# Optimization experiments

Measured on AMD Instinct MI355X. Metric: run time of the kernel, lower is better.

## Reference

```python
import jax, jax.numpy as jnp
import numpy as np
import math

IN_F = 2048
INTER_F = 8192
OUT_F = 2048
STRIPE = 256
N_STRIPES = INTER_F // STRIPE
EPS = 1e-7
BETA = 0.99
STEPS = 1000.0
THRESH_LR_SCALE = 1.0 * math.sqrt(IN_F)


def setup_inputs() -> dict:
    key = jax.random.key(0)
    ks = jax.random.split(key, 8)
    x = jax.random.normal(ks[0], (2, 1024, IN_F), dtype=jnp.float32)
    gate_weight = jax.random.normal(ks[1], (IN_F, INTER_F), dtype=jnp.float32) / math.sqrt(IN_F)
    gate_bias = jnp.zeros((INTER_F,), dtype=jnp.float32)
    # thresholds ~ threshold_init scale so the mask is non-trivially sparse
    gate_thresholds = jax.random.uniform(ks[2], (N_STRIPES, IN_F), dtype=jnp.float32) * (0.1 / THRESH_LR_SCALE) * 20.0
    med = jax.random.normal(ks[3], (IN_F,), dtype=jnp.float32) * 0.01
    aad = jax.random.uniform(ks[4], (IN_F,), dtype=jnp.float32) + 0.5
    up_weight = jax.random.normal(ks[5], (IN_F, INTER_F), dtype=jnp.float32) * 0.02
    up_bias = jnp.zeros((INTER_F,), dtype=jnp.float32)
    down_weight = jax.random.normal(ks[6], (OUT_F, INTER_F), dtype=jnp.float32) / math.sqrt(INTER_F)
    down_bias = jnp.zeros((OUT_F,), dtype=jnp.float32)
    return dict(x=x, gate_weight=gate_weight, gate_bias=gate_bias,
                gate_thresholds=gate_thresholds, med=med, aad=aad,
                up_weight=up_weight, up_bias=up_bias,
                down_weight=down_weight, down_bias=down_bias)


def _cwic_linear(xf, weight, bias, thresholds, med, aad):
    # eval-mode CWICLinear. xf: [T, I]
    debiaser = 1.0 / (EPS + (1.0 - BETA ** STEPS))
    mu = med * debiaser                                   # [I]
    std = aad * debiaser / math.sqrt(2.0 * math.pi)      # [I]
    thr = thresholds * std[None, :] * THRESH_LR_SCALE     # [N, I]
    xd = xf - mu[None, :]                                 # [T, I]
    mask = (jnp.abs(xd)[:, None, :] > thr[None]).astype(xf.dtype)  # [T, N, I]
    xm = xd[:, None, :] * mask + mu[None, None, :]        # [T, N, I]
    w = weight.T.reshape(N_STRIPES, STRIPE, IN_F)          # [N, S, I]
    y = jnp.einsum('nsi,tni->tns', w, xm).reshape(-1, INTER_F) + bias[None, :]
    active = STRIPE * mask.reshape(xf.shape[0], -1).sum(axis=-1)  # [T]
    dense = jnp.full_like(active, STRIPE * N_STRIPES * IN_F)
    return y, dense, active


def reference(x, gate_weight, gate_bias, gate_thresholds, med, aad,
              up_weight, up_bias, down_weight, down_bias):
    B, T, I = x.shape
    xf = x.reshape(-1, I)
    g, dense, active = _cwic_linear(xf, gate_weight, gate_bias, gate_thresholds, med, aad)
    up = xf @ up_weight + up_bias[None, :]                 # Conv1D: x @ W + b
    h = jax.nn.silu(g) * up                                # [BT, inter]
    y = h @ down_weight.T + down_bias[None, :]             # nn.Linear
    return (y.reshape(B, T, OUT_F), dense.reshape(B, T), active.reshape(B, T))
```

## Files before the change

kernel.cpp:

```cpp
#include <hip/hip_runtime.h>
#include <math.h>
#include <stdint.h>

typedef __bf16 bf16_t;
typedef __bf16 bf16x8 __attribute__((ext_vector_type(8)));
typedef __bf16 bf16x4 __attribute__((ext_vector_type(4)));
typedef float f32x4 __attribute__((ext_vector_type(4)));
typedef short s16x8 __attribute__((ext_vector_type(8)));

#define TOKS 2048
#define INF 2048
#define JNF 8192
#define ONF 2048


template <int ROWS, int NT>
__device__ __forceinline__ void stage_async_t(const bf16_t* __restrict__ src, size_t ld,
                                              bf16_t* lds, int tid) {
  constexpr int IT = ROWS * 8 / NT;
#pragma unroll
  for (int r = 0; r < IT; ++r) {
    int c = r * NT + tid;
    int row = c >> 3;
    int kq = (c & 7) ^ (row & 7);
    const bf16_t* g = src + (size_t)row * ld + kq * 8;
    bf16_t* l = lds + (size_t)(r * NT + (tid & ~63)) * 8;
    __builtin_amdgcn_global_load_lds((const __attribute__((address_space(1))) void*)g,
                                     (__attribute__((address_space(3))) void*)l,
                                     16, 0, 0);
  }
}

__device__ __forceinline__ bf16x8 frag_ld64(const bf16_t* lds, int row, int kq) {
  int slot = kq ^ (row & 7);
  return *(const bf16x8*)&lds[row * 64 + slot * 8];
}


__global__ __launch_bounds__(256) void prep_mu_thr(
    const float* __restrict__ med, const float* __restrict__ aad,
    const float* __restrict__ gth, float debiaser,
    float* __restrict__ mu, float* __restrict__ thr, bf16_t* __restrict__ thrb) {
  int gid = blockIdx.x * 256 + threadIdx.x;
  if (gid < INF) mu[gid] = med[gid] * debiaser;
  int i = gid & (INF - 1);
  float stdv = aad[i] * debiaser / 2.5066282746310002f;
  float tv = gth[gid] * stdv * 45.254833995939045f;
  thr[gid] = tv;
  thrb[gid] = (bf16_t)tv;
}

__global__ __launch_bounds__(256) void prep_x_count(
    const float* __restrict__ x, const float* __restrict__ mu,
    const float* __restrict__ thr,
    bf16_t* __restrict__ xb, bf16_t* __restrict__ xdb,
    float* __restrict__ dense, float* __restrict__ active) {
  int t = blockIdx.x;
  int tid = threadIdx.x;
  int i0 = tid * 8;
  const float* xrow = x + (size_t)t * INF;
  f32x4 x0 = *(const f32x4*)&xrow[i0];
  f32x4 x1 = *(const f32x4*)&xrow[i0 + 4];
  f32x4 m0 = *(const f32x4*)&mu[i0];
  f32x4 m1 = *(const f32x4*)&mu[i0 + 4];
  f32x4 d0 = x0 - m0, d1 = x1 - m1;
  bf16x8 ox, od;
  ox[0] = (bf16_t)x0[0]; ox[1] = (bf16_t)x0[1]; ox[2] = (bf16_t)x0[2]; ox[3] = (bf16_t)x0[3];
  ox[4] = (bf16_t)x1[0]; ox[5] = (bf16_t)x1[1]; ox[6] = (bf16_t)x1[2]; ox[7] = (bf16_t)x1[3];
  od[0] = (bf16_t)d0[0]; od[1] = (bf16_t)d0[1]; od[2] = (bf16_t)d0[2]; od[3] = (bf16_t)d0[3];
  od[4] = (bf16_t)d1[0]; od[5] = (bf16_t)d1[1]; od[6] = (bf16_t)d1[2]; od[7] = (bf16_t)d1[3];
  *(bf16x8*)&xb[(size_t)t * INF + i0] = ox;
  *(bf16x8*)&xdb[(size_t)t * INF + i0] = od;
  f32x4 a0, a1;
  a0[0] = fabsf(d0[0]); a0[1] = fabsf(d0[1]); a0[2] = fabsf(d0[2]); a0[3] = fabsf(d0[3]);
  a1[0] = fabsf(d1[0]); a1[1] = fabsf(d1[1]); a1[2] = fabsf(d1[2]); a1[3] = fabsf(d1[3]);
  int cnt = 0;
#pragma unroll 4
  for (int n = 0; n < 32; ++n) {
    f32x4 t0 = *(const f32x4*)&thr[(n << 11) + i0];
    f32x4 t1 = *(const f32x4*)&thr[(n << 11) + i0 + 4];
    cnt += (a0[0] > t0[0]) + (a0[1] > t0[1]) + (a0[2] > t0[2]) + (a0[3] > t0[3]);
    cnt += (a1[0] > t1[0]) + (a1[1] > t1[1]) + (a1[2] > t1[2]) + (a1[3] > t1[3]);
  }
  for (int off = 32; off; off >>= 1) cnt += __shfl_down(cnt, off);
  __shared__ int red[4];
  int wv = tid >> 6;
  if ((tid & 63) == 0) red[wv] = cnt;
  __syncthreads();
  if (tid == 0) {
    int tot = red[0] + red[1] + red[2] + red[3];
    active[t] = 256.0f * (float)tot;
    dense[t] = 16777216.0f;
  }
}

__global__ __launch_bounds__(256) void transpose_cast_dual(
    const float* __restrict__ src0, bf16_t* __restrict__ dst0,
    const float* __restrict__ src1, bf16_t* __restrict__ dst1) {
  const float* src = blockIdx.z ? src1 : src0;
  bf16_t* dst = blockIdx.z ? dst1 : dst0;
  __shared__ float tile[32][33];
  int j0 = blockIdx.x * 32;
  int i0 = blockIdx.y * 32;
  int r = threadIdx.x >> 3;
  int c = (threadIdx.x & 7) * 4;
  f32x4 v = *(const f32x4*)&src[(i0 + r) * JNF + j0 + c];
  tile[r][c] = v[0]; tile[r][c + 1] = v[1]; tile[r][c + 2] = v[2]; tile[r][c + 3] = v[3];
  __syncthreads();
  bf16x4 o;
  o[0] = (bf16_t)tile[c + 0][r];
  o[1] = (bf16_t)tile[c + 1][r];
  o[2] = (bf16_t)tile[c + 2][r];
  o[3] = (bf16_t)tile[c + 3][r];
  *(bf16x4*)&dst[(j0 + r) * INF + i0 + c] = o;
}

__global__ __launch_bounds__(256) void cast_bf16(
    const float* __restrict__ src, bf16_t* __restrict__ dst) {
  int idx = (blockIdx.x * 256 + threadIdx.x) * 8;
  f32x4 a = *(const f32x4*)&src[idx];
  f32x4 b = *(const f32x4*)&src[idx + 4];
  bf16x8 o;
  o[0] = (bf16_t)a[0]; o[1] = (bf16_t)a[1]; o[2] = (bf16_t)a[2]; o[3] = (bf16_t)a[3];
  o[4] = (bf16_t)b[0]; o[5] = (bf16_t)b[1]; o[6] = (bf16_t)b[2]; o[7] = (bf16_t)b[3];
  *(bf16x8*)&dst[idx] = o;
}

__global__ __launch_bounds__(256) void c_from_gwT(
    const bf16_t* __restrict__ gwT, const float* __restrict__ mu,
    const float* __restrict__ gb, float* __restrict__ c) {
  int j = blockIdx.x * 4 + (threadIdx.x >> 6);
  int lane = threadIdx.x & 63;
  float s = 0.f;
#pragma unroll
  for (int it = 0; it < 4; ++it) {
    int i = it * 512 + lane * 8;
    bf16x8 w = *(const bf16x8*)&gwT[(size_t)j * INF + i];
    f32x4 m0 = *(const f32x4*)&mu[i];
    f32x4 m1 = *(const f32x4*)&mu[i + 4];
    s += (float)w[0] * m0[0] + (float)w[1] * m0[1] + (float)w[2] * m0[2] + (float)w[3] * m0[3];
    s += (float)w[4] * m1[0] + (float)w[5] * m1[1] + (float)w[6] * m1[2] + (float)w[7] * m1[3];
  }
  for (int off = 32; off; off >>= 1) s += __shfl_down(s, off);
  if (lane == 0) c[j] = gb[j] + s;
}


__global__ __launch_bounds__(512) void gate_gemm(
    const bf16_t* __restrict__ xdb, const bf16_t* __restrict__ thrb,
    const bf16_t* __restrict__ gwT, const float* __restrict__ cj,
    bf16_t* __restrict__ g) {
  __shared__ bf16_t Al[128 * 64];
  __shared__ bf16_t Bl[256 * 64];
  int tid = threadIdx.x;
  int t0 = blockIdx.y * 128;
  int j0 = blockIdx.x * 256;
  int n = blockIdx.x;
  int lane = tid & 63;
  int wv = tid >> 6;
  int wr = (wv & 1) * 64;
  int wc = (wv >> 1) * 64;
  int m16 = lane & 15, q = lane >> 4;
  f32x4 acc[4][4] = {};
  const s16x8 absmask = {0x7FFF, 0x7FFF, 0x7FFF, 0x7FFF, 0x7FFF, 0x7FFF, 0x7FFF, 0x7FFF};
  for (int k0 = 0; k0 < INF; k0 += 64) {
    stage_async_t<256, 512>(gwT + (size_t)j0 * INF + k0, INF, Bl, tid);
#pragma unroll
    for (int r = 0; r < 2; ++r) {
      int c = r * 512 + tid;
      int row = c >> 3;
      int slot = c & 7;
      int kq = slot ^ (row & 7);
      s16x8 a = *(const s16x8*)&xdb[(size_t)(t0 + row) * INF + k0 + kq * 8];
      s16x8 t = *(const s16x8*)&thrb[n * INF + k0 + kq * 8];
      s16x8 m = (s16x8)((t - (a & absmask)) >> 15);
      *(s16x8*)&Al[row * 64 + slot * 8] = a & m;
    }
    __syncthreads();
#pragma unroll
    for (int s = 0; s < 2; ++s) {
      bf16x8 af[4], bf[4];
#pragma unroll
      for (int mi = 0; mi < 4; ++mi) af[mi] = frag_ld64(Al, wr + mi * 16 + m16, s * 4 + q);
#pragma unroll
      for (int ni = 0; ni < 4; ++ni) bf[ni] = frag_ld64(Bl, wc + ni * 16 + m16, s * 4 + q);
#pragma unroll
      for (int mi = 0; mi < 4; ++mi)
#pragma unroll
        for (int ni = 0; ni < 4; ++ni)
          acc[mi][ni] = __builtin_amdgcn_mfma_f32_16x16x32_bf16(af[mi], bf[ni], acc[mi][ni], 0, 0, 0);
    }
    __syncthreads();
  }
#pragma unroll
  for (int mi = 0; mi < 4; ++mi)
#pragma unroll
    for (int ni = 0; ni < 4; ++ni) {
      int col = j0 + wc + ni * 16 + m16;
      float cadd = cj[col];
#pragma unroll
      for (int r = 0; r < 4; ++r) {
        int row = t0 + wr + mi * 16 + q * 4 + r;
        g[(size_t)row * JNF + col] = (bf16_t)(acc[mi][ni][r] + cadd);
      }
    }
}


__global__ __launch_bounds__(256) void up_gemm(
    const bf16_t* __restrict__ xb, const bf16_t* __restrict__ upT,
    const float* __restrict__ ub, const bf16_t* __restrict__ g,
    bf16_t* __restrict__ h) {
  __shared__ bf16_t Al[128 * 64];
  __shared__ bf16_t Bl[128 * 64];
  int tid = threadIdx.x;
  int t0 = blockIdx.y * 128;
  int j0 = blockIdx.x * 128;
  int lane = tid & 63;
  int wv = tid >> 6;
  int wr = (wv & 1) * 64;
  int wc = (wv >> 1) * 64;
  int m16 = lane & 15, q = lane >> 4;
  f32x4 acc[4][4] = {};
  for (int k0 = 0; k0 < INF; k0 += 64) {
    stage_async_t<128, 256>(xb + (size_t)t0 * INF + k0, INF, Al, tid);
    stage_async_t<128, 256>(upT + (size_t)j0 * INF + k0, INF, Bl, tid);
    __syncthreads();
#pragma unroll
    for (int s = 0; s < 2; ++s) {
      bf16x8 af[4], bf[4];
#pragma unroll
      for (int mi = 0; mi < 4; ++mi) af[mi] = frag_ld64(Al, wr + mi * 16 + m16, s * 4 + q);
#pragma unroll
      for (int ni = 0; ni < 4; ++ni) bf[ni] = frag_ld64(Bl, wc + ni * 16 + m16, s * 4 + q);
#pragma unroll
      for (int mi = 0; mi < 4; ++mi)
#pragma unroll
        for (int ni = 0; ni < 4; ++ni)
          acc[mi][ni] = __builtin_amdgcn_mfma_f32_16x16x32_bf16(af[mi], bf[ni], acc[mi][ni], 0, 0, 0);
    }
    __syncthreads();
  }
#pragma unroll
  for (int mi = 0; mi < 4; ++mi)
#pragma unroll
    for (int ni = 0; ni < 4; ++ni) {
      int col = j0 + wc + ni * 16 + m16;
      float bias = ub[col];
#pragma unroll
      for (int r = 0; r < 4; ++r) {
        int row = t0 + wr + mi * 16 + q * 4 + r;
        float upv = acc[mi][ni][r] + bias;
        float gv = (float)g[(size_t)row * JNF + col];
        float hv = (gv / (1.f + expf(-gv))) * upv;
        h[(size_t)row * JNF + col] = (bf16_t)hv;
      }
    }
}

__global__ __launch_bounds__(256) void down_gemm(
    const bf16_t* __restrict__ h, const bf16_t* __restrict__ dwb,
    float* __restrict__ part) {
  __shared__ bf16_t Al[128 * 64];
  __shared__ bf16_t Bl[128 * 64];
  int tid = threadIdx.x;
  int t0 = blockIdx.y * 128;
  int o0 = blockIdx.x * 128;
  int kz = blockIdx.z * 2048;
  int lane = tid & 63;
  int wv = tid >> 6;
  int wr = (wv & 1) * 64;
  int wc = (wv >> 1) * 64;
  int m16 = lane & 15, q = lane >> 4;
  f32x4 acc[4][4] = {};
  for (int k0 = kz; k0 < kz + 2048; k0 += 64) {
    stage_async_t<128, 256>(h + (size_t)t0 * JNF + k0, JNF, Al, tid);
    stage_async_t<128, 256>(dwb + (size_t)o0 * JNF + k0, JNF, Bl, tid);
    __syncthreads();
#pragma unroll
    for (int s = 0; s < 2; ++s) {
      bf16x8 af[4], bf[4];
#pragma unroll
      for (int mi = 0; mi < 4; ++mi) af[mi] = frag_ld64(Al, wr + mi * 16 + m16, s * 4 + q);
#pragma unroll
      for (int ni = 0; ni < 4; ++ni) bf[ni] = frag_ld64(Bl, wc + ni * 16 + m16, s * 4 + q);
#pragma unroll
      for (int mi = 0; mi < 4; ++mi)
#pragma unroll
        for (int ni = 0; ni < 4; ++ni)
          acc[mi][ni] = __builtin_amdgcn_mfma_f32_16x16x32_bf16(af[mi], bf[ni], acc[mi][ni], 0, 0, 0);
    }
    __syncthreads();
  }
  float* dst = part + (size_t)blockIdx.z * (TOKS * ONF);
#pragma unroll
  for (int mi = 0; mi < 4; ++mi)
#pragma unroll
    for (int ni = 0; ni < 4; ++ni) {
      int col = o0 + wc + ni * 16 + m16;
#pragma unroll
      for (int r = 0; r < 4; ++r) {
        int row = t0 + wr + mi * 16 + q * 4 + r;
        dst[(size_t)row * ONF + col] = acc[mi][ni][r];
      }
    }
}

__global__ __launch_bounds__(256) void down_reduce(
    const float* __restrict__ part, const float* __restrict__ db,
    float* __restrict__ y) {
  int idx = (blockIdx.x * 256 + threadIdx.x) * 4;
  f32x4 a = *(const f32x4*)&part[idx];
  f32x4 b = *(const f32x4*)&part[idx + 4194304];
  f32x4 c = *(const f32x4*)&part[idx + 2 * 4194304];
  f32x4 d = *(const f32x4*)&part[idx + 3 * 4194304];
  f32x4 bias = *(const f32x4*)&db[idx & (ONF - 1)];
  *(f32x4*)&y[idx] = a + b + c + d + bias;
}


extern "C" void kernel_launch(void* const* d_in, const int* in_sizes, int n_in,
                              void* d_out, int out_size, void* d_ws, size_t ws_size,
                              hipStream_t stream) {
  (void)in_sizes; (void)n_in; (void)out_size; (void)ws_size;
  const float* x   = (const float*)d_in[0];
  const float* gw  = (const float*)d_in[1];
  const float* gb  = (const float*)d_in[2];
  const float* gth = (const float*)d_in[3];
  const float* med = (const float*)d_in[4];
  const float* aad = (const float*)d_in[5];
  const float* uw  = (const float*)d_in[6];
  const float* ub  = (const float*)d_in[7];
  const float* dw  = (const float*)d_in[8];
  const float* db  = (const float*)d_in[9];

  float* out = (float*)d_out;
  float* y = out;
  float* dense = out + 4194304;
  float* active = dense + 2048;

  char* ws = (char*)d_ws;
  float*  mu   = (float*)(ws + 0);
  float*  thr  = (float*)(ws + 8192);
  bf16_t* thrb = (bf16_t*)(ws + 270336);
  float*  cj   = (float*)(ws + 401408);
  bf16_t* xb   = (bf16_t*)(ws + 434176);
  bf16_t* xdb  = (bf16_t*)(ws + 8822784);
  bf16_t* gwT  = (bf16_t*)(ws + 17211392);
  bf16_t* upT  = (bf16_t*)(ws + 50765824);
  bf16_t* dwb  = (bf16_t*)(ws + 84320256);
  bf16_t* hb   = (bf16_t*)(ws + 117874688);
  float*  part = (float*)(ws + 151429120);
  bf16_t* gb16 = (bf16_t*)part;

  float debiaser = (float)(1.0 / (1e-7 + (1.0 - pow(0.99, 1000.0))));

  prep_mu_thr<<<256, 256, 0, stream>>>(med, aad, gth, debiaser, mu, thr, thrb);
  prep_x_count<<<2048, 256, 0, stream>>>(x, mu, thr, xb, xdb, dense, active);
  transpose_cast_dual<<<dim3(256, 64, 2), 256, 0, stream>>>(gw, gwT, uw, upT);
  cast_bf16<<<8192, 256, 0, stream>>>(dw, dwb);
  c_from_gwT<<<2048, 256, 0, stream>>>(gwT, mu, gb, cj);
  gate_gemm<<<dim3(32, 16), 512, 0, stream>>>(xdb, thrb, gwT, cj, gb16);
  up_gemm<<<dim3(64, 16), 256, 0, stream>>>(xb, upT, ub, gb16, hb);
  down_gemm<<<dim3(16, 16, 4), 256, 0, stream>>>(hb, dwb, part);
  down_reduce<<<4096, 256, 0, stream>>>(part, db, y);
}
```

Before: 556.0 us.

## Unify GEMMs into double-buffered 256x256 tile kernel with phased barriers

The gate, up and down GEMMs are replaced by one templated 256x256-tile kernel with 512 threads. It double-buffers A and B in LDS so the next K-tile loads while the current one is computed, and splits each tile into four phases with barriers and s_setprio around the MFMA bursts. The larger tile raises data reuse per block, but it uses 128KB of LDS, which allows one block per CU. The grids shrink to 256 blocks for each GEMM, so the GPU's CUs may be underfilled and tail effects may worsen.

```diff
diff --git a/kernel.cpp b/kernel.cpp
--- a/kernel.cpp
+++ b/kernel.cpp
@@ -146,164 +146,168 @@
 }
 
 
-__global__ __launch_bounds__(512) void gate_gemm(
-    const bf16_t* __restrict__ xdb, const bf16_t* __restrict__ thrb,
-    const bf16_t* __restrict__ gwT, const float* __restrict__ cj,
-    bf16_t* __restrict__ g) {
-  __shared__ bf16_t Al[128 * 64];
-  __shared__ bf16_t Bl[256 * 64];
+template <int MODE>
+__global__ __launch_bounds__(512) void gemm256(
+    const bf16_t* __restrict__ Ag, const bf16_t* __restrict__ Bg,
+    const bf16_t* __restrict__ thrv, const float* __restrict__ cvec,
+    const bf16_t* __restrict__ gmat, bf16_t* __restrict__ outb,
+    float* __restrict__ outf) {
+  constexpr int NTILES = 32;
+  constexpr size_t LD = (MODE == 1) ? (size_t)JNF : (size_t)INF;
+  __shared__ bf16_t Al[2][256 * 64];
+  __shared__ bf16_t Bl[2][256 * 64];
   int tid = threadIdx.x;
-  int t0 = blockIdx.y * 128;
-  int j0 = blockIdx.x * 256;
-  int n = blockIdx.x;
   int lane = tid & 63;
   int wv = tid >> 6;
-  int wr = (wv & 1) * 64;
-  int wc = (wv >> 1) * 64;
+  int wm = wv >> 2;
+  int wn = wv & 3;
   int m16 = lane & 15, q = lane >> 4;
-  f32x4 acc[4][4] = {};
-  const s16x8 absmask = {0x7FFF, 0x7FFF, 0x7FFF, 0x7FFF, 0x7FFF, 0x7FFF, 0x7FFF, 0x7FFF};
-  for (int k0 = 0; k0 < INF; k0 += 64) {
-    stage_async_t<256, 512>(gwT + (size_t)j0 * INF + k0, INF, Bl, tid);
-#pragma unroll
-    for (int r = 0; r < 2; ++r) {
-      int c = r * 512 + tid;
-      int row = c >> 3;
-      int slot = c & 7;
-      int kq = slot ^ (row & 7);
-      s16x8 a = *(const s16x8*)&xdb[(size_t)(t0 + row) * INF + k0 + kq * 8];
-      s16x8 t = *(const s16x8*)&thrb[n * INF + k0 + kq * 8];
-      s16x8 m = (s16x8)((t - (a & absmask)) >> 15);
-      *(s16x8*)&Al[row * 64 + slot * 8] = a & m;
+  int t0 = blockIdx.y * 256;
+  int j0 = blockIdx.x * 256;
+  int kbeg = (MODE == 1) ? blockIdx.z * 2048 : 0;
+  const bf16_t* Arow = Ag + (size_t)t0 * LD + kbeg;
+  const bf16_t* Brow = Bg + (size_t)j0 * LD + kbeg;
+  const bf16_t* Tn = (MODE == 2) ? thrv + (size_t)blockIdx.x * INF : (const bf16_t*)nullptr;
+  const s16x8 ABS = {0x7FFF, 0x7FFF, 0x7FFF, 0x7FFF, 0x7FFF, 0x7FFF, 0x7FFF, 0x7FFF};
+
+  f32x4 acc[8][4] = {};
+
+  stage_async_t<256, 512>(Brow, LD, Bl[0], tid);
+  if constexpr (MODE == 2) {
+    s16x8 av0[4], tv0[4];
+#pragma unroll
+    for (int r2 = 0; r2 < 4; ++r2) {
+      int ch = r2 * 512 + tid;
+      int row = ch >> 3;
+      int kq = (ch & 7) ^ (row & 7);
+      av0[r2] = *(const s16x8*)&Arow[(size_t)row * LD + kq * 8];
+      tv0[r2] = *(const s16x8*)&Tn[kq * 8];
     }
-    __syncthreads();
-#pragma unroll
-    for (int s = 0; s < 2; ++s) {
-      bf16x8 af[4], bf[4];
-#pragma unroll
-      for (int mi = 0; mi < 4; ++mi) af[mi] = frag_ld64(Al, wr + mi * 16 + m16, s * 4 + q);
-#pragma unroll
-      for (int ni = 0; ni < 4; ++ni) bf[ni] = frag_ld64(Bl, wc + ni * 16 + m16, s * 4 + q);
-#pragma unroll
-      for (int mi = 0; mi < 4; ++mi)
+#pragma unroll
+    for (int r2 = 0; r2 < 4; ++r2) {
+      int ch = r2 * 512 + tid;
+      int row = ch >> 3;
+      int sl = ch & 7;
+      s16x8 m = (s16x8)((tv0[r2] - (av0[r2] & ABS)) >> 15);
+      *(s16x8*)&Al[0][row * 64 + sl * 8] = av0[r2] & m;
+    }
+  } else {
+    stage_async_t<256, 512>(Arow, LD, Al[0], tid);
+  }
+  asm volatile("s_waitcnt vmcnt(0) lgkmcnt(0)" ::: "memory");
+  __builtin_amdgcn_s_barrier();
+
+  for (int u = 0; u < NTILES; ++u) {
+    int c = u & 1;
+    const bf16_t* Ab = Al[c];
+    const bf16_t* Bb = Bl[c];
+    bf16x8 bfr[4][2];
+    s16x8 av[4], tv[4];
+#pragma unroll
+    for (int p = 0; p < 4; ++p) {
+      if (p == 0) {
+        if (u + 1 < NTILES) {
+          stage_async_t<256, 512>(Brow + (u + 1) * 64, LD, Bl[c ^ 1], tid);
+          if constexpr (MODE == 2) {
+            int k0 = (u + 1) * 64;
+#pragma unroll
+            for (int r2 = 0; r2 < 4; ++r2) {
+              int ch = r2 * 512 + tid;
+              int row = ch >> 3;
+              int kq = (ch & 7) ^ (row & 7);
+              av[r2] = *(const s16x8*)&Arow[(size_t)row * LD + k0 + kq * 8];
+              tv[r2] = *(const s16x8*)&Tn[k0 + kq * 8];
+            }
+          } else {
+            stage_async_t<256, 512>(Arow + (u + 1) * 64, LD, Al[c ^ 1], tid);
+          }
+        }
 #pragma unroll
         for (int ni = 0; ni < 4; ++ni)
-          acc[mi][ni] = __builtin_amdgcn_mfma_f32_16x16x32_bf16(af[mi], bf[ni], acc[mi][ni], 0, 0, 0);
+#pragma unroll
+          for (int ks = 0; ks < 2; ++ks)
+            bfr[ni][ks] = frag_ld64(Bb, wn * 64 + ni * 16 + m16, ks * 4 + q);
+      }
+      bf16x8 af[2][2];
+#pragma unroll
+      for (int mi2 = 0; mi2 < 2; ++mi2)
+#pragma unroll
+        for (int ks = 0; ks < 2; ++ks)
+          af[mi2][ks] = frag_ld64(Ab, wm * 128 + (p * 2 + mi2) * 16 + m16, ks * 4 + q);
+      if constexpr (MODE == 2) {
+        if (p == 2 && u + 1 < NTILES) {
+#pragma unroll
+          for (int r2 = 0; r2 < 4; ++r2) {
+            int ch = r2 * 512 + tid;
+            int row = ch >> 3;
+            int sl = ch & 7;
+            s16x8 m = (s16x8)((tv[r2] - (av[r2] & ABS)) >> 15);
+            *(s16x8*)&Al[c ^ 1][row * 64 + sl * 8] = av[r2] & m;
+          }
+        }
+      }
+      __builtin_amdgcn_s_barrier();
+      __builtin_amdgcn_s_setprio(1);
+#pragma unroll
+      for (int mi2 = 0; mi2 < 2; ++mi2)
+#pragma unroll
+        for (int ni = 0; ni < 4; ++ni)
+#pragma unroll
+          for (int ks = 0; ks < 2; ++ks)
+            acc[p * 2 + mi2][ni] = __builtin_amdgcn_mfma_f32_16x16x32_bf16(
+                af[mi2][ks], bfr[ni][ks], acc[p * 2 + mi2][ni], 0, 0, 0);
+      __builtin_amdgcn_s_setprio(0);
+      if (p < 3) __builtin_amdgcn_s_barrier();
     }
-    __syncthreads();
-  }
-#pragma unroll
-  for (int mi = 0; mi < 4; ++mi)
-#pragma unroll
-    for (int ni = 0; ni < 4; ++ni) {
-      int col = j0 + wc + ni * 16 + m16;
-      float cadd = cj[col];
-#pragma unroll
-      for (int r = 0; r < 4; ++r) {
-        int row = t0 + wr + mi * 16 + q * 4 + r;
-        g[(size_t)row * JNF + col] = (bf16_t)(acc[mi][ni][r] + cadd);
-      }
-    }
-}
-
-
-__global__ __launch_bounds__(256) void up_gemm(
-    const bf16_t* __restrict__ xb, const bf16_t* __restrict__ upT,
-    const float* __restrict__ ub, const bf16_t* __restrict__ g,
-    bf16_t* __restrict__ h) {
-  __shared__ bf16_t Al[128 * 64];
-  __shared__ bf16_t Bl[128 * 64];
-  int tid = threadIdx.x;
-  int t0 = blockIdx.y * 128;
-  int j0 = blockIdx.x * 128;
-  int lane = tid & 63;
-  int wv = tid >> 6;
-  int wr = (wv & 1) * 64;
-  int wc = (wv >> 1) * 64;
-  int m16 = lane & 15, q = lane >> 4;
-  f32x4 acc[4][4] = {};
-  for (int k0 = 0; k0 < INF; k0 += 64) {
-    stage_async_t<128, 256>(xb + (size_t)t0 * INF + k0, INF, Al, tid);
-    stage_async_t<128, 256>(upT + (size_t)j0 * INF + k0, INF, Bl, tid);
-    __syncthreads();
-#pragma unroll
-    for (int s = 0; s < 2; ++s) {
-      bf16x8 af[4], bf[4];
-#pragma unroll
-      for (int mi = 0; mi < 4; ++mi) af[mi] = frag_ld64(Al, wr + mi * 16 + m16, s * 4 + q);
-#pragma unroll
-      for (int ni = 0; ni < 4; ++ni) bf[ni] = frag_ld64(Bl, wc + ni * 16 + m16, s * 4 + q);
-#pragma unroll
-      for (int mi = 0; mi < 4; ++mi)
-#pragma unroll
-        for (int ni = 0; ni < 4; ++ni)
-          acc[mi][ni] = __builtin_amdgcn_mfma_f32_16x16x32_bf16(af[mi], bf[ni], acc[mi][ni], 0, 0, 0);
-    }
-    __syncthreads();
-  }
-#pragma unroll
-  for (int mi = 0; mi < 4; ++mi)
-#pragma unroll
-    for (int ni = 0; ni < 4; ++ni) {
-      int col = j0 + wc + ni * 16 + m16;
-      float bias = ub[col];
-#pragma unroll
-      for (int r = 0; r < 4; ++r) {
-        int row = t0 + wr + mi * 16 + q * 4 + r;
-        float upv = acc[mi][ni][r] + bias;
-        float gv = (float)g[(size_t)row * JNF + col];
-        float hv = (gv / (1.f + expf(-gv))) * upv;
-        h[(size_t)row * JNF + col] = (bf16_t)hv;
-      }
-    }
-}
-
-__global__ __launch_bounds__(256) void down_gemm(
-    const bf16_t* __restrict__ h, const bf16_t* __restrict__ dwb,
-    float* __restrict__ part) {
-  __shared__ bf16_t Al[128 * 64];
-  __shared__ bf16_t Bl[128 * 64];
-  int tid = threadIdx.x;
-  int t0 = blockIdx.y * 128;
-  int o0 = blockIdx.x * 128;
-  int kz = blockIdx.z * 2048;
-  int lane = tid & 63;
-  int wv = tid >> 6;
-  int wr = (wv & 1) * 64;
-  int wc = (wv >> 1) * 64;
-  int m16 = lane & 15, q = lane >> 4;
-  f32x4 acc[4][4] = {};
-  for (int k0 = kz; k0 < kz + 2048; k0 += 64) {
-    stage_async_t<128, 256>(h + (size_t)t0 * JNF + k0, JNF, Al, tid);
-    stage_async_t<128, 256>(dwb + (size_t)o0 * JNF + k0, JNF, Bl, tid);
-    __syncthreads();
-#pragma unroll
-    for (int s = 0; s < 2; ++s) {
-      bf16x8 af[4], bf[4];
-#pragma unroll
-      for (int mi = 0; mi < 4; ++mi) af[mi] = frag_ld64(Al, wr + mi * 16 + m16, s * 4 + q);
-#pragma unroll
-      for (int ni = 0; ni < 4; ++ni) bf[ni] = frag_ld64(Bl, wc + ni * 16 + m16, s * 4 + q);
-#pragma unroll
-      for (int mi = 0; mi < 4; ++mi)
-#pragma unroll
-        for (int ni = 0; ni < 4; ++ni)
-          acc[mi][ni] = __builtin_amdgcn_mfma_f32_16x16x32_bf16(af[mi], bf[ni], acc[mi][ni], 0, 0, 0);
-    }
-    __syncthreads();
-  }
-  float* dst = part + (size_t)blockIdx.z * (TOKS * ONF);
-#pragma unroll
-  for (int mi = 0; mi < 4; ++mi)
-#pragma unroll
-    for (int ni = 0; ni < 4; ++ni) {
-      int col = o0 + wc + ni * 16 + m16;
-#pragma unroll
-      for (int r = 0; r < 4; ++r) {
-        int row = t0 + wr + mi * 16 + q * 4 + r;
-        dst[(size_t)row * ONF + col] = acc[mi][ni][r];
-      }
-    }
+    asm volatile("s_waitcnt vmcnt(0) lgkmcnt(0)" ::: "memory");
+    __builtin_amdgcn_s_barrier();
+  }
+
+  int cb = j0 + wn * 64;
+  int rb = t0 + wm * 128;
+  if constexpr (MODE == 1) {
+    float* dst = outf + (size_t)blockIdx.z * ((size_t)TOKS * ONF);
+#pragma unroll
+    for (int mi = 0; mi < 8; ++mi)
+#pragma unroll
+      for (int ni = 0; ni < 4; ++ni) {
+        int col = cb + ni * 16 + m16;
+#pragma unroll
+        for (int r = 0; r < 4; ++r) {
+          int row = rb + mi * 16 + q * 4 + r;
+          dst[(size_t)row * ONF + col] = acc[mi][ni][r];
+        }
+      }
+  } else if constexpr (MODE == 0) {
+#pragma unroll
+    for (int mi = 0; mi < 8; ++mi)
+#pragma unroll
+      for (int ni = 0; ni < 4; ++ni) {
+        int col = cb + ni * 16 + m16;
+        float bias = cvec[col];
+#pragma unroll
+        for (int r = 0; r < 4; ++r) {
+          int row = rb + mi * 16 + q * 4 + r;
+          float upv = acc[mi][ni][r] + bias;
+          float gv = (float)gmat[(size_t)row * JNF + col];
+          float hv = (gv / (1.f + expf(-gv))) * upv;
+          outb[(size_t)row * JNF + col] = (bf16_t)hv;
+        }
+      }
+  } else {
+#pragma unroll
+    for (int mi = 0; mi < 8; ++mi)
+#pragma unroll
+      for (int ni = 0; ni < 4; ++ni) {
+        int col = cb + ni * 16 + m16;
+        float cadd = cvec[col];
+#pragma unroll
+        for (int r = 0; r < 4; ++r) {
+          int row = rb + mi * 16 + q * 4 + r;
+          outb[(size_t)row * JNF + col] = (bf16_t)(acc[mi][ni][r] + cadd);
+        }
+      }
+  }
 }
 
 __global__ __launch_bounds__(256) void down_reduce(
@@ -360,8 +364,8 @@
   transpose_cast_dual<<<dim3(256, 64, 2), 256, 0, stream>>>(gw, gwT, uw, upT);
   cast_bf16<<<8192, 256, 0, stream>>>(dw, dwb);
   c_from_gwT<<<2048, 256, 0, stream>>>(gwT, mu, gb, cj);
-  gate_gemm<<<dim3(32, 16), 512, 0, stream>>>(xdb, thrb, gwT, cj, gb16);
-  up_gemm<<<dim3(64, 16), 256, 0, stream>>>(xb, upT, ub, gb16, hb);
-  down_gemm<<<dim3(16, 16, 4), 256, 0, stream>>>(hb, dwb, part);
+  gemm256<2><<<dim3(32, 8), 512, 0, stream>>>(xdb, gwT, thrb, cj, nullptr, gb16, nullptr);
+  gemm256<0><<<dim3(32, 8), 512, 0, stream>>>(xb, upT, nullptr, ub, gb16, hb, nullptr);
+  gemm256<1><<<dim3(8, 8, 4), 512, 0, stream>>>(hb, dwb, nullptr, nullptr, nullptr, nullptr, part);
   down_reduce<<<4096, 256, 0, stream>>>(part, db, y);
 }
```

After: 570.1 us. 1.03x slower.
